# Optimization experiments

Measured on AMD Instinct MI355X. Metric: run time of the kernel, lower is better.

## Reference

```python
import jax, jax.numpy as jnp
import numpy as np

B, N, C = 8, 1024, 768
DIM_HEAD = 32
NUM_HEADS = C // DIM_HEAD  # 24


def setup_inputs() -> dict:
    key = jax.random.key(0)
    ks = jax.random.split(key, 6)
    s = 0.02
    return {
        "x": jax.random.normal(ks[0], (B, N, C), dtype=jnp.float32),
        "shared_rel_pos": jax.random.normal(ks[1], (NUM_HEADS, N, N), dtype=jnp.float32),
        "Wqkv": jax.random.normal(ks[2], (3 * C, C), dtype=jnp.float32) * s,
        "bqkv": jax.random.normal(ks[3], (3 * C,), dtype=jnp.float32) * s,
        "Wproj": jax.random.normal(ks[4], (C, C), dtype=jnp.float32) * s,
        "bproj": jax.random.normal(ks[5], (C,), dtype=jnp.float32) * s,
    }


def reference(x, shared_rel_pos, Wqkv, bqkv, Wproj, bproj):
    b, n, c = x.shape
    h, dh = NUM_HEADS, DIM_HEAD
    scale = dh ** -0.5
    # qkv projection: [B,N,3C] -> view as [B,N,H,3*dh] (head_first layout)
    qkv = (jnp.einsum('bnc,oc->bno', x, Wqkv) + bqkv).reshape(b, n, h, 3 * dh)
    qkv = jnp.transpose(qkv, (0, 2, 1, 3))          # [B,H,N,3*dh]
    q, k, v = jnp.split(qkv, 3, axis=-1)            # each [B,H,N,dh]
    attn = jnp.einsum('bhqd,bhkd->bhqk', q * scale, k)  # [B,H,N,N]
    attn = attn + shared_rel_pos[None]              # broadcast bias [H,N,N]
    attn = jax.nn.softmax(attn, axis=-1)
    out = jnp.einsum('bhqk,bhkd->bhqd', attn, v)    # [B,H,N,dh]
    out = jnp.transpose(out, (0, 2, 1, 3)).reshape(b, n, h * dh)
    return jnp.einsum('bnc,oc->bno', out, Wproj) + bproj
```

## Files before the change

### kernel.cpp

```cpp
#include <hip/hip_runtime.h>

typedef __bf16 bf16_t;
typedef __bf16 bf16x8 __attribute__((ext_vector_type(8)));
typedef __bf16 bf16x4 __attribute__((ext_vector_type(4)));
typedef float f32x4 __attribute__((ext_vector_type(4)));

#define MFMA16(a, b, c) __builtin_amdgcn_mfma_f32_16x16x32_bf16(a, b, c, 0, 0, 0)

__device__ __forceinline__ void g2l16(const void* g, void* l) {
  __builtin_amdgcn_global_load_lds(
      (__attribute__((address_space(1))) void*)g,
      (__attribute__((address_space(3))) void*)l, 16, 0, 0);
}

__global__ void cvt_f32_bf16(const float* __restrict__ in, bf16_t* __restrict__ out, int n4) {
  int i = blockIdx.x * blockDim.x + threadIdx.x;
  if (i >= n4) return;
  const float4 v = ((const float4*)in)[i];
  bf16x4 o;
  o[0] = (bf16_t)v.x; o[1] = (bf16_t)v.y; o[2] = (bf16_t)v.z; o[3] = (bf16_t)v.w;
  ((bf16x4*)out)[i] = o;
}

__global__ void transpose_v(const bf16_t* __restrict__ Vb, bf16_t* __restrict__ Vtb) {
  __shared__ bf16_t T[64][40];
  const int bh = blockIdx.y, s0 = blockIdx.x * 64;
  const int r = threadIdx.x >> 2, c8 = (threadIdx.x & 3) * 8;
  const bf16x8 v = *(const bf16x8*)(Vb + ((size_t)bh * 1024 + s0 + r) * 32 + c8);
#pragma unroll
  for (int j = 0; j < 8; ++j) T[r][c8 + j] = v[j];
  __syncthreads();
  const int d = threadIdx.x >> 3, q8 = (threadIdx.x & 7) * 8;
  bf16x8 o;
#pragma unroll
  for (int j = 0; j < 8; ++j) o[j] = T[q8 + j][d];
  *(bf16x8*)(Vtb + ((size_t)bh * 32 + d) * 1024 + s0 + q8) = o;
}

template <int MODE>
__global__ __launch_bounds__(256, 2) void gemm_bt(
    const bf16_t* __restrict__ A, const bf16_t* __restrict__ Bw,
    const float* __restrict__ bias, float* __restrict__ Cout,
    bf16_t* __restrict__ Qb, bf16_t* __restrict__ Kb, bf16_t* __restrict__ Vb,
    int M, int N, int K) {
  __shared__ bf16_t As[128 * 32];
  __shared__ bf16_t Bs[128 * 32];
  const int tid = threadIdx.x;
  const int wave = tid >> 6, lane = tid & 63, quad = lane >> 4, lr = lane & 15;
  const int bm = blockIdx.x * 128, bn = blockIdx.y * 128;
  const int wm = (wave >> 1) * 64, wn = (wave & 1) * 64;

  f32x4 acc[4][4] = {};

  const bf16_t* Ag;
  size_t strideA64;
  if (MODE == 0) {
    Ag = A + (size_t)(bm + (tid >> 2)) * K + (tid & 3) * 8;
    strideA64 = (size_t)64 * K;
  } else {
    const int rr = bm + (tid >> 2);
    const int bidx = rr >> 10, seq = rr & 1023;
    Ag = A + ((size_t)bidx * 24 * 1024 + seq) * 32 + (tid & 3) * 8;
    strideA64 = (size_t)64 * 32;
  }
  const bf16_t* Bg = Bw + (size_t)(bn + (tid >> 2)) * K + (tid & 3) * 8;
  bf16_t* As0 = As + tid * 8;
  bf16_t* Bs0 = Bs + tid * 8;
  const size_t strideB64 = (size_t)64 * K;

  for (int k0 = 0; k0 < K; k0 += 32) {
    const size_t aoff = (MODE == 0) ? (size_t)k0 : (size_t)(k0 >> 5) * 32768;
    __syncthreads();
    g2l16(Ag + aoff, As0);
    g2l16(Ag + strideA64 + aoff, As0 + 2048);
    g2l16(Bg + k0, Bs0);
    g2l16(Bg + strideB64 + k0, Bs0 + 2048);
    __syncthreads();
    bf16x8 af[4], bfr[4];
#pragma unroll
    for (int i = 0; i < 4; ++i)
      af[i] = *(const bf16x8*)(As + (wm + i * 16 + lr) * 32 + quad * 8);
#pragma unroll
    for (int j = 0; j < 4; ++j)
      bfr[j] = *(const bf16x8*)(Bs + (wn + j * 16 + lr) * 32 + quad * 8);
#pragma unroll
    for (int i = 0; i < 4; ++i)
#pragma unroll
      for (int j = 0; j < 4; ++j)
        acc[i][j] = MFMA16(af[i], bfr[j], acc[i][j]);
  }

#pragma unroll
  for (int i = 0; i < 4; ++i) {
    const int row = bm + wm + i * 16 + quad * 4;
#pragma unroll
    for (int j = 0; j < 4; ++j) {
      const int col = bn + wn + j * 16 + lr;
      const float bb = bias[col];
#pragma unroll
      for (int r = 0; r < 4; ++r) {
        const float v = acc[i][j][r] + bb;
        const int rr = row + r;
        if (MODE == 1) {
          Cout[(size_t)rr * N + col] = v;
        } else {
          const int b = rr >> 10, seq = rr & 1023;
          const int head = col / 96, w = col % 96;
          const int bh = b * 24 + head;
          if (w < 32) {
            Qb[((size_t)bh * 1024 + seq) * 32 + w] = (bf16_t)(v * 0.17677669529663687f);
          } else if (w < 64) {
            Kb[((size_t)bh * 1024 + seq) * 32 + (w - 32)] = (bf16_t)v;
          } else {
            Vb[((size_t)bh * 1024 + seq) * 32 + (w - 64)] = (bf16_t)v;
          }
        }
      }
    }
  }
}

__global__ __launch_bounds__(256, 4) void attn_flash(
    const bf16_t* __restrict__ Qb, const bf16_t* __restrict__ Kb,
    const bf16_t* __restrict__ Vtb, const float* __restrict__ rel,
    bf16_t* __restrict__ Ob) {
  __shared__ bf16_t Ps[4][16 * 132];

  const int tid = threadIdx.x;
  const int wave = tid >> 6, lane = tid & 63, quad = lane >> 4, lr = lane & 15;

  const int flat = blockIdx.x;
  const int xcd = flat & 7, slot = flat >> 3;
  const int pair = xcd + 8 * (slot >> 4);
  const int qi = slot & 15;
  const int b = pair / 24, h = pair % 24;
  const int bh = b * 24 + h;
  const int q0 = qi * 64 + wave * 16;
  const float LOG2E = 1.44269504f;

  const bf16x8 qf = *(const bf16x8*)(Qb + ((size_t)bh * 1024 + q0 + lr) * 32 + quad * 8);

  f32x4 o_acc[2] = {};
  float l_i[4] = {0.f, 0.f, 0.f, 0.f};

  const float* relg = rel + ((size_t)h * 1024 + q0 + quad * 4) * 1024 + lr;
  const bf16_t* Kg = Kb + (size_t)bh * 1024 * 32;
  const bf16_t* Vg = Vtb + (size_t)bh * 32 * 1024;
  bf16_t* Pw = &Ps[wave][0];

  auto body = [&](int kt) {
    float bv[8][4];
    const float* rb = relg + kt;
#pragma unroll
    for (int jt = 0; jt < 8; ++jt)
#pragma unroll
      for (int r = 0; r < 4; ++r)
        bv[jt][r] = rb[(size_t)r * 1024 + jt * 16] * LOG2E;

    const bf16_t* Kbase = Kg + (size_t)kt * 32;
    const bf16_t* Vbase = Vg + kt;

    f32x4 s[8];
    const f32x4 zz = {0.f, 0.f, 0.f, 0.f};
#pragma unroll
    for (int jt = 0; jt < 8; ++jt) {
      const bf16x8 kf = *(const bf16x8*)(Kbase + (size_t)(jt * 16 + lr) * 32 + quad * 8);
      s[jt] = MFMA16(qf, kf, zz);
    }
#pragma unroll
    for (int jt = 0; jt < 8; ++jt)
#pragma unroll
      for (int r = 0; r < 4; ++r)
        s[jt][r] = exp2f(fmaf(s[jt][r], LOG2E, bv[jt][r]));

#pragma unroll
    for (int jt = 0; jt < 8; ++jt)
#pragma unroll
      for (int r = 0; r < 4; ++r)
        Pw[(quad * 4 + r) * 132 + jt * 16 + lr] = (bf16_t)s[jt][r];

#pragma unroll
    for (int r = 0; r < 4; ++r) {
      float sm = 0.f;
#pragma unroll
      for (int jt = 0; jt < 8; ++jt) sm += s[jt][r];
#pragma unroll
      for (int off = 1; off < 16; off <<= 1) sm += __shfl_xor(sm, off, 16);
      l_i[r] += sm;
    }

#pragma unroll
    for (int ks = 0; ks < 4; ++ks) {
      const bf16x8 pf = *(const bf16x8*)(Pw + lr * 132 + ks * 32 + quad * 8);
#pragma unroll
      for (int nt = 0; nt < 2; ++nt) {
        const bf16x8 vf = *(const bf16x8*)(Vbase + (size_t)(nt * 16 + lr) * 1024 + ks * 32 + quad * 8);
        o_acc[nt] = MFMA16(pf, vf, o_acc[nt]);
      }
    }
  };

  for (int kt = 0; kt < 1024; kt += 256) {
    body(kt);
    body(kt + 128);
  }

  float inv_l[4];
#pragma unroll
  for (int r = 0; r < 4; ++r) inv_l[r] = 1.0f / l_i[r];
#pragma unroll
  for (int nt = 0; nt < 2; ++nt)
#pragma unroll
    for (int r = 0; r < 4; ++r) {
      const int seq = q0 + quad * 4 + r;
      Ob[((size_t)bh * 1024 + seq) * 32 + nt * 16 + lr] = (bf16_t)(o_acc[nt][r] * inv_l[r]);
    }
}

extern "C" void kernel_launch(void* const* d_in, const int* in_sizes, int n_in,
                              void* d_out, int out_size, void* d_ws, size_t ws_size,
                              hipStream_t stream) {
  const float* x = (const float*)d_in[0];
  const float* rel = (const float*)d_in[1];
  const float* Wqkv = (const float*)d_in[2];
  const float* bqkv = (const float*)d_in[3];
  const float* Wproj = (const float*)d_in[4];
  const float* bproj = (const float*)d_in[5];
  float* out = (float*)d_out;

  char* ws = (char*)d_ws;
  bf16_t* xb = (bf16_t*)ws;     ws += (size_t)8192 * 768 * 2;
  bf16_t* wqkvb = (bf16_t*)ws;  ws += (size_t)2304 * 768 * 2;
  bf16_t* wprojb = (bf16_t*)ws; ws += (size_t)768 * 768 * 2;
  bf16_t* Qb = (bf16_t*)ws;     ws += (size_t)192 * 1024 * 32 * 2;
  bf16_t* Kb = (bf16_t*)ws;     ws += (size_t)192 * 1024 * 32 * 2;
  bf16_t* Vb = (bf16_t*)ws;     ws += (size_t)192 * 1024 * 32 * 2;
  bf16_t* Vtb = (bf16_t*)ws;    ws += (size_t)192 * 1024 * 32 * 2;
  bf16_t* Ob = xb;

  cvt_f32_bf16<<<(8192 * 768 / 4 + 255) / 256, 256, 0, stream>>>(x, xb, 8192 * 768 / 4);
  cvt_f32_bf16<<<(2304 * 768 / 4 + 255) / 256, 256, 0, stream>>>(Wqkv, wqkvb, 2304 * 768 / 4);
  cvt_f32_bf16<<<(768 * 768 / 4 + 255) / 256, 256, 0, stream>>>(Wproj, wprojb, 768 * 768 / 4);

  gemm_bt<0><<<dim3(64, 18), 256, 0, stream>>>(xb, wqkvb, bqkv, nullptr,
                                               Qb, Kb, Vb, 8192, 2304, 768);
  transpose_v<<<dim3(16, 192), 256, 0, stream>>>(Vb, Vtb);
  attn_flash<<<dim3(3072), 256, 0, stream>>>(Qb, Kb, Vtb, rel, Ob);
  gemm_bt<1><<<dim3(64, 6), 256, 0, stream>>>(Ob, wprojb, bproj, out,
                                              nullptr, nullptr, nullptr, 8192, 768, 768);
}
```

Before: 399.5 us.

## Pre-permute relative position bias to bf16 with MFMA-friendly layout

```diff
diff --git a/kernel.cpp b/kernel.cpp
--- a/kernel.cpp
+++ b/kernel.cpp
@@ -20,6 +20,25 @@
   bf16x4 o;
   o[0] = (bf16_t)v.x; o[1] = (bf16_t)v.y; o[2] = (bf16_t)v.z; o[3] = (bf16_t)v.w;
   ((bf16x4*)out)[i] = o;
+}
+
+__global__ void permute_rel(const float* __restrict__ rel, bf16_t* __restrict__ relp) {
+  __shared__ float row[1024];
+  const size_t base = (size_t)blockIdx.x * 1024;
+  const int t = threadIdx.x;
+  *(float4*)(row + t * 4) = *(const float4*)(rel + base + t * 4);
+  __syncthreads();
+  const float LOG2E = 1.44269504f;
+  const int o0 = t * 4;
+  bf16x4 v;
+#pragma unroll
+  for (int j = 0; j < 4; ++j) {
+    const int o = o0 + j;
+    const int kb = o >> 7, rem = o & 127;
+    const int lr = rem >> 3, jt = rem & 7;
+    v[j] = (bf16_t)(row[kb * 128 + jt * 16 + lr] * LOG2E);
+  }
+  *(bf16x4*)(relp + base + o0) = v;
 }
 
 __global__ void transpose_v(const bf16_t* __restrict__ Vb, bf16_t* __restrict__ Vtb) {
@@ -122,7 +141,7 @@
 
 __global__ __launch_bounds__(256, 4) void attn_flash(
     const bf16_t* __restrict__ Qb, const bf16_t* __restrict__ Kb,
-    const bf16_t* __restrict__ Vtb, const float* __restrict__ rel,
+    const bf16_t* __restrict__ Vtb, const bf16_t* __restrict__ relp,
     bf16_t* __restrict__ Ob) {
   __shared__ bf16_t Ps[4][16 * 132];
 
@@ -143,19 +162,16 @@
   f32x4 o_acc[2] = {};
   float l_i[4] = {0.f, 0.f, 0.f, 0.f};
 
-  const float* relg = rel + ((size_t)h * 1024 + q0 + quad * 4) * 1024 + lr;
+  const bf16_t* relg = relp + ((size_t)h * 1024 + q0 + quad * 4) * 1024 + lr * 8;
   const bf16_t* Kg = Kb + (size_t)bh * 1024 * 32;
   const bf16_t* Vg = Vtb + (size_t)bh * 32 * 1024;
   bf16_t* Pw = &Ps[wave][0];
 
   auto body = [&](int kt) {
-    float bv[8][4];
-    const float* rb = relg + kt;
-#pragma unroll
-    for (int jt = 0; jt < 8; ++jt)
-#pragma unroll
-      for (int r = 0; r < 4; ++r)
-        bv[jt][r] = rb[(size_t)r * 1024 + jt * 16] * LOG2E;
+    bf16x8 bw[4];
+    const bf16_t* rb = relg + kt;
+#pragma unroll
+    for (int r = 0; r < 4; ++r) bw[r] = *(const bf16x8*)(rb + (size_t)r * 1024);
 
     const bf16_t* Kbase = Kg + (size_t)kt * 32;
     const bf16_t* Vbase = Vg + kt;
@@ -171,7 +187,7 @@
     for (int jt = 0; jt < 8; ++jt)
 #pragma unroll
       for (int r = 0; r < 4; ++r)
-        s[jt][r] = exp2f(fmaf(s[jt][r], LOG2E, bv[jt][r]));
+        s[jt][r] = exp2f(fmaf(s[jt][r], LOG2E, (float)bw[r][jt]));
 
 #pragma unroll
     for (int jt = 0; jt < 8; ++jt)
@@ -236,16 +252,18 @@
   bf16_t* Kb = (bf16_t*)ws;     ws += (size_t)192 * 1024 * 32 * 2;
   bf16_t* Vb = (bf16_t*)ws;     ws += (size_t)192 * 1024 * 32 * 2;
   bf16_t* Vtb = (bf16_t*)ws;    ws += (size_t)192 * 1024 * 32 * 2;
+  bf16_t* relp = (bf16_t*)ws;   ws += (size_t)24 * 1024 * 1024 * 2;
   bf16_t* Ob = xb;
 
   cvt_f32_bf16<<<(8192 * 768 / 4 + 255) / 256, 256, 0, stream>>>(x, xb, 8192 * 768 / 4);
   cvt_f32_bf16<<<(2304 * 768 / 4 + 255) / 256, 256, 0, stream>>>(Wqkv, wqkvb, 2304 * 768 / 4);
   cvt_f32_bf16<<<(768 * 768 / 4 + 255) / 256, 256, 0, stream>>>(Wproj, wprojb, 768 * 768 / 4);
+  permute_rel<<<dim3(24 * 1024), 256, 0, stream>>>(rel, relp);
 
   gemm_bt<0><<<dim3(64, 18), 256, 0, stream>>>(xb, wqkvb, bqkv, nullptr,
                                                Qb, Kb, Vb, 8192, 2304, 768);
   transpose_v<<<dim3(16, 192), 256, 0, stream>>>(Vb, Vtb);
-  attn_flash<<<dim3(3072), 256, 0, stream>>>(Qb, Kb, Vtb, rel, Ob);
+  attn_flash<<<dim3(3072), 256, 0, stream>>>(Qb, Kb, Vtb, relp, Ob);
   gemm_bt<1><<<dim3(64, 6), 256, 0, stream>>>(Ob, wprojb, bproj, out,
                                               nullptr, nullptr, nullptr, 8192, 768, 768);
 }
```

Result: slower. 413.7 us (+3.5%).
